# Optimization experiments

Hardware: AMD Instinct MI355X
Metric: run time of the kernel (lower is better)

## Reference

```python
import jax, jax.numpy as jnp
import numpy as np

# Static module configuration (RT-DETR defaults, 640x640 input pyramid)
SPATIAL_SHAPES = ((80, 80), (40, 40), (20, 20))
N_HEADS = 8
N_LEVELS = 3
N_POINTS = 4
D_MODEL = 256
HEAD_DIM = D_MODEL // N_HEADS
OFFSET_SCALE = 0.5
LP = N_LEVELS * N_POINTS


def setup_inputs() -> dict:
    key = jax.random.key(0)
    ks = jax.random.split(key, 10)
    B, Q = 16, 300
    S = sum(h * w for h, w in SPATIAL_SHAPES)  # 8400

    def w(k, shape, scale=0.02):
        return jax.random.normal(k, shape, jnp.float32) * scale

    return {
        "hidden_states": jax.random.normal(ks[0], (B, Q, D_MODEL), jnp.float32),
        "encoder_hidden_states": jax.random.normal(ks[1], (B, S, D_MODEL), jnp.float32),
        # (cx, cy, w, h) boxes in (0,1); 4-coordinate RTDETRv2 path
        "reference_points": jax.random.uniform(ks[2], (B, Q, 1, 4), jnp.float32, 0.1, 0.9),
        "w_value": w(ks[3], (D_MODEL, D_MODEL)),
        "b_value": jnp.zeros((D_MODEL,), jnp.float32),
        "w_offsets": w(ks[4], (N_HEADS * LP * 2, D_MODEL)),
        "b_offsets": w(ks[5], (N_HEADS * LP * 2,), 0.5),
        "w_attn": w(ks[6], (N_HEADS * LP, D_MODEL)),
        "b_attn": jnp.zeros((N_HEADS * LP,), jnp.float32),
        "w_out": w(ks[7], (D_MODEL, D_MODEL)),
        "b_out": jnp.zeros((D_MODEL,), jnp.float32),
    }


def _bilinear_sample(img, gx, gy):
    """grid_sample(mode=bilinear, padding_mode=zeros, align_corners=False).
    img: [N, C, H, W]; gx, gy: [N, Q, P] absolute pixel coords (already W*loc-0.5).
    Returns [N, Q, P, C]."""
    N, C, H, W = img.shape
    x0 = jnp.floor(gx)
    y0 = jnp.floor(gy)
    x1 = x0 + 1.0
    y1 = y0 + 1.0
    wx1 = gx - x0
    wx0 = 1.0 - wx1
    wy1 = gy - y0
    wy0 = 1.0 - wy1
    b = jnp.arange(N)[:, None, None]

    def gather(ix, iy):
        valid = (ix >= 0) & (ix < W) & (iy >= 0) & (iy < H)
        ixc = jnp.clip(ix, 0, W - 1).astype(jnp.int32)
        iyc = jnp.clip(iy, 0, H - 1).astype(jnp.int32)
        v = img[b, :, iyc, ixc]  # [N,Q,P,C]
        return v * valid[..., None].astype(img.dtype)

    return (gather(x0, y0) * (wx0 * wy0)[..., None]
            + gather(x1, y0) * (wx1 * wy0)[..., None]
            + gather(x0, y1) * (wx0 * wy1)[..., None]
            + gather(x1, y1) * (wx1 * wy1)[..., None])


def _msda_v2(hidden_states, encoder_hidden_states, reference_points,
             w_value, b_value, w_offsets, b_offsets, w_attn, b_attn, w_out, b_out):
    B, Q, _ = hidden_states.shape
    S = encoder_hidden_states.shape[1]

    value = (encoder_hidden_states @ w_value.T + b_value).reshape(B, S, N_HEADS, HEAD_DIM)
    offsets = (hidden_states @ w_offsets.T + b_offsets).reshape(B, Q, N_HEADS, LP, 2)
    attn = jax.nn.softmax(
        (hidden_states @ w_attn.T + b_attn).reshape(B, Q, N_HEADS, LP), axis=-1)

    # n_points_scale = [1/P]*L*P; 4-coordinate reference points (cx,cy,w,h)
    n_points_scale = jnp.float32(1.0 / N_POINTS)
    offset = offsets * n_points_scale * reference_points[:, :, None, :, 2:] * OFFSET_SCALE
    loc = reference_points[:, :, None, :, :2] + offset  # [B,Q,H,LP,2] in (0,1)

    # head-major value: [B*H, hd, S]
    v = value.transpose(0, 2, 3, 1).reshape(B * N_HEADS, HEAD_DIM, S)
    grids = loc.transpose(0, 2, 1, 3, 4).reshape(B * N_HEADS, Q, LP, 2)

    sampled = []
    start = 0
    for lvl, (H, W) in enumerate(SPATIAL_SHAPES):
        vl = v[:, :, start:start + H * W].reshape(B * N_HEADS, HEAD_DIM, H, W)
        g = grids[:, :, lvl * N_POINTS:(lvl + 1) * N_POINTS, :]
        # torch: grid = 2*loc-1 with align_corners=False -> pixel = loc*W - 0.5
        gx = g[..., 0] * W - 0.5
        gy = g[..., 1] * H - 0.5
        sampled.append(_bilinear_sample(vl, gx, gy))  # [B*H, Q, P, hd]
        start += H * W

    sv = jnp.concatenate(sampled, axis=2)  # [B*H, Q, LP, hd]
    aw = attn.transpose(0, 2, 1, 3).reshape(B * N_HEADS, Q, LP, 1)
    out = (sv * aw).sum(axis=2)  # [B*H, Q, hd]
    out = out.reshape(B, N_HEADS, Q, HEAD_DIM).transpose(0, 2, 1, 3).reshape(B, Q, D_MODEL)
    return out @ w_out.T + b_out


def reference(hidden_states, encoder_hidden_states, reference_points,
              w_value, b_value, w_offsets, b_offsets, w_attn, b_attn, w_out, b_out):
    return _msda_v2(hidden_states, encoder_hidden_states, reference_points,
                    w_value, b_value, w_offsets, b_offsets, w_attn, b_attn, w_out, b_out)
```

## Files before the change

kernel.cpp:

```cpp
#include <hip/hip_runtime.h>


typedef __attribute__((ext_vector_type(8))) short short8;
typedef __attribute__((ext_vector_type(4))) short short4v;
typedef __attribute__((ext_vector_type(4))) float f32x4;

__device__ __forceinline__ unsigned short f2bf(float f) {
    union { float f; unsigned int i; } v; v.f = f;
    unsigned int r = v.i + 0x7FFFu + ((v.i >> 16) & 1u);
    return (unsigned short)(r >> 16);
}
__device__ __forceinline__ float bf2f(unsigned short u) {
    union { unsigned int i; float f; } v;
    v.i = ((unsigned int)u) << 16;
    return v.f;
}
__device__ __forceinline__ short8 cvt8(const float* p) {
    f32x4 x = *(const f32x4*)p;
    f32x4 y = *(const f32x4*)(p + 4);
    short8 r;
#pragma unroll
    for (int q = 0; q < 4; ++q) {
        r[q]     = (short)f2bf(x[q]);
        r[q + 4] = (short)f2bf(y[q]);
    }
    return r;
}
__device__ __forceinline__ void barrier_lgkm() {
    asm volatile("s_waitcnt lgkmcnt(0)\n\ts_barrier" ::: "memory");
}

__global__ __launch_bounds__(256) void prep_kernel(
    const float* __restrict__ wv, const float* __restrict__ wo,
    const float* __restrict__ w_off, const float* __restrict__ w_attn,
    short8* __restrict__ wv_s, short8* __restrict__ wo_s, short8* __restrict__ wp_s)
{
    const int blk = blockIdx.x, tid = threadIdx.x;
    if (blk < 64) {
        const float* W = (blk < 32) ? wv : wo;
        short8* out    = (blk < 32) ? wv_s : wo_s;
        int s   = ((blk & 31) << 8) + tid;
        int kcb = s >> 10, sl = s & 1023;
        int n = ((sl >> 6) << 4) + (sl & 15);
        int k = (kcb << 5) + (((sl >> 4) & 3) << 3);
        out[s] = cvt8(W + n * 256 + k);
    } else {
        int s   = ((blk - 64) << 8) + tid;
        int kcb = s / 1152, sl = s - kcb * 1152;
        int n = ((sl >> 6) << 4) + (sl & 15);
        int k = (kcb << 5) + (((sl >> 4) & 3) << 3);
        const float* p = (n < 192) ? (w_off + (size_t)n * 256 + k)
                                   : (w_attn + (size_t)(n - 192) * 256 + k);
        wp_s[s] = cvt8(p);
    }
}

__global__ __launch_bounds__(256) void gemm128(
    const float* __restrict__ A,
    const short8* __restrict__ Wswz,
    const float* __restrict__ bias,
    unsigned short* __restrict__ C)
{
    __shared__ short8 lb[1024];
    const int tid  = threadIdx.x;
    const int wave = tid >> 6;
    const int lane = tid & 63;
    const int row0 = (blockIdx.x >> 1) * 128;
    const int colt = blockIdx.x & 1;
    const int mq   = wave >> 1;
    const int nq   = wave & 1;

    f32x4 acc[4][4];
#pragma unroll
    for (int i = 0; i < 4; ++i)
#pragma unroll
        for (int j = 0; j < 4; ++j) acc[i][j] = (f32x4){0.f, 0.f, 0.f, 0.f};

    const int sa0 = tid, sa1 = tid + 256;
    const int am0 = row0 + ((sa0 >> 6) << 4) + (sa0 & 15);
    const int ak0 = ((sa0 >> 4) & 3) << 3;
    const int am1 = row0 + ((sa1 >> 6) << 4) + (sa1 & 15);
    const int ak1 = ((sa1 >> 4) & 3) << 3;

    for (int kcb = 0; kcb < 8; ++kcb) {
        const int kc = kcb << 5;
        barrier_lgkm();
        lb[sa0] = cvt8(A + (size_t)am0 * 256 + kc + ak0);
        lb[sa1] = cvt8(A + (size_t)am1 * 256 + kc + ak1);
        const short8* wsrc = Wswz + (kcb << 10) + (colt << 9);
        lb[512 + tid]       = wsrc[tid];
        lb[768 + tid]       = wsrc[tid + 256];
        barrier_lgkm();

        short8 af[4], bf[4];
#pragma unroll
        for (int i = 0; i < 4; ++i) af[i] = lb[((mq << 2) + i) * 64 + lane];
#pragma unroll
        for (int j = 0; j < 4; ++j) bf[j] = lb[512 + ((nq << 2) + j) * 64 + lane];
#pragma unroll
        for (int i = 0; i < 4; ++i)
#pragma unroll
            for (int j = 0; j < 4; ++j)
                acc[i][j] = __builtin_amdgcn_mfma_f32_16x16x32_bf16(af[i], bf[j], acc[i][j], 0, 0, 0);
    }

    const int ncol = lane & 15;
    const int rsub = (lane >> 4) << 2;
#pragma unroll
    for (int i = 0; i < 4; ++i) {
        const int rb = row0 + ((mq << 2) + i) * 16 + rsub;
#pragma unroll
        for (int j = 0; j < 4; ++j) {
            const int n = (colt << 7) + ((nq << 2) + j) * 16 + ncol;
            const float bv = bias[n];
#pragma unroll
            for (int r = 0; r < 4; ++r)
                C[(size_t)(rb + r) * 256 + n] = f2bf(acc[i][j][r] + bv);
        }
    }
}

template <bool A_BF16, bool OUT_BF16>
__global__ __launch_bounds__(256) void gemm_nt(
    const void* __restrict__ Av,
    const short8* __restrict__ Wswz,
    const float* __restrict__ bias,
    void* __restrict__ Cv)
{
    __shared__ short8 lb[1024];
    const int tid  = threadIdx.x;
    const int wave = tid >> 6;
    const int lane = tid & 63;
    const int row0 = (blockIdx.x >> 1) * 64 + wave * 16;
    const int colt = blockIdx.x & 1;

    f32x4 acc[8];
#pragma unroll
    for (int t = 0; t < 8; ++t) acc[t] = (f32x4){0.f, 0.f, 0.f, 0.f};

    const int am = row0 + (lane & 15);
    const int kq = (lane >> 4) << 3;

    const unsigned short* Ab = (const unsigned short*)Av;
    const float*          Af = (const float*)Av;

    short8 acur[2], anext[2];
#pragma unroll
    for (int kk = 0; kk < 2; ++kk) {
        if (A_BF16) acur[kk] = *(const short8*)(Ab + (size_t)am * 256 + (kk << 5) + kq);
        else        acur[kk] = cvt8(Af + (size_t)am * 256 + (kk << 5) + kq);
    }

    for (int st = 0; st < 4; ++st) {
        barrier_lgkm();
#pragma unroll
        for (int i = 0; i < 4; ++i) {
            int s  = tid + (i << 8);
            int kk = s >> 9, r = s & 511;
            lb[s] = Wswz[(((st << 1) + kk) << 10) + (colt << 9) + r];
        }
        barrier_lgkm();

        if (st < 3) {
            int kc = (st + 1) << 6;
#pragma unroll
            for (int kk = 0; kk < 2; ++kk) {
                if (A_BF16) anext[kk] = *(const short8*)(Ab + (size_t)am * 256 + kc + (kk << 5) + kq);
                else        anext[kk] = cvt8(Af + (size_t)am * 256 + kc + (kk << 5) + kq);
            }
        }

#pragma unroll
        for (int t = 0; t < 8; ++t) {
            short8 b0 = lb[t * 64 + lane];
            acc[t] = __builtin_amdgcn_mfma_f32_16x16x32_bf16(acur[0], b0, acc[t], 0, 0, 0);
            short8 b1 = lb[512 + t * 64 + lane];
            acc[t] = __builtin_amdgcn_mfma_f32_16x16x32_bf16(acur[1], b1, acc[t], 0, 0, 0);
        }
        acur[0] = anext[0];
        acur[1] = anext[1];
    }

    const int ncol = lane & 15;
    const int rb   = row0 + ((lane >> 4) << 2);
#pragma unroll
    for (int t = 0; t < 8; ++t) {
        int n = (colt << 7) + (t << 4) + ncol;
        float bv = bias[n];
#pragma unroll
        for (int r = 0; r < 4; ++r) {
            float v = acc[t][r] + bv;
            if (OUT_BF16)
                ((unsigned short*)Cv)[(size_t)(rb + r) * 256 + n] = f2bf(v);
            else
                ((float*)Cv)[(size_t)(rb + r) * 256 + n] = v;
        }
    }
}

#define LGS 296
__global__ __launch_bounds__(256) void proj_gemm(
    const float* __restrict__ hidden,
    const short8* __restrict__ Wswz,
    const float* __restrict__ b_off, const float* __restrict__ b_attn,
    const float* __restrict__ refp,
    float* __restrict__ attnw, float* __restrict__ locw)
{
    __shared__ char smem[32 * LGS * 4];
    short8* lb = (short8*)smem;
    float*  lg = (float*)smem;

    const int tid  = threadIdx.x;
    const int wave = tid >> 6;
    const int lane = tid & 63;
    const int rq0  = blockIdx.x * 32;
    const int rg   = wave >> 1;
    const int ts   = (wave & 1) * 9;
    const int row0 = rq0 + rg * 16;

    f32x4 acc[9];
#pragma unroll
    for (int t = 0; t < 9; ++t) acc[t] = (f32x4){0.f, 0.f, 0.f, 0.f};

    const int am = row0 + (lane & 15);
    const int kq = (lane >> 4) << 3;

    for (int kcb = 0; kcb < 8; ++kcb) {
        __syncthreads();
#pragma unroll
        for (int i = 0; i < 5; ++i) {
            int s = tid + (i << 8);
            if (s < 1152) lb[s] = Wswz[kcb * 1152 + s];
        }
        __syncthreads();

        short8 a = cvt8(hidden + (size_t)am * 256 + (kcb << 5) + kq);
#pragma unroll
        for (int t = 0; t < 9; ++t)
            acc[t] = __builtin_amdgcn_mfma_f32_16x16x32_bf16(a, lb[(ts + t) * 64 + lane], acc[t], 0, 0, 0);
    }

    __syncthreads();
    const int ncol = lane & 15;
    const int rb   = rg * 16 + ((lane >> 4) << 2);
#pragma unroll
    for (int t = 0; t < 9; ++t) {
        int n = (ts + t) * 16 + ncol;
        float bv = (n < 192) ? b_off[n] : b_attn[n - 192];
#pragma unroll
        for (int r = 0; r < 4; ++r)
            lg[(rb + r) * LGS + n] = acc[t][r] + bv;
    }
    __syncthreads();

    {
        int r = tid >> 3, h = tid & 7;
        const float* lrow = lg + r * LGS + 192 + h * 12;
        float m = -1e30f;
#pragma unroll
        for (int p = 0; p < 12; ++p) m = fmaxf(m, lrow[p]);
        float e[12], sum = 0.f;
#pragma unroll
        for (int p = 0; p < 12; ++p) { e[p] = __expf(lrow[p] - m); sum += e[p]; }
        float inv = 1.f / sum;
        float* ao = attnw + (size_t)(rq0 + r) * 96 + h * 12;
#pragma unroll
        for (int p = 0; p < 12; ++p) ao[p] = e[p] * inv;
    }
    if (tid < 192) {
        int xy = tid & 1;
        for (int r = 0; r < 32; ++r) {
            int rq = rq0 + r;
            float rc  = refp[(size_t)rq * 4 + xy];
            float rwh = refp[(size_t)rq * 4 + 2 + xy];
            locw[(size_t)rq * 192 + tid] = rc + lg[r * LGS + tid] * 0.125f * rwh;
        }
    }
}

__global__ __launch_bounds__(256) void sample_kernel(
    const unsigned short* __restrict__ value,
    const float* __restrict__ attnw, const float* __restrict__ locw,
    unsigned short* __restrict__ sampled)
{
    const int rq0 = blockIdx.x << 2;
    const int tid = threadIdx.x;

    __shared__ int4   soff[4][96];
    __shared__ float4 swt[4][96];

    for (int it = tid; it < 384; it += 256) {
        int rsub = it / 96;
        int idx  = it - rsub * 96;
        int rq   = rq0 + rsub;
        int b    = rq / 300;
        int h  = idx / 12, lp = idx - h * 12;
        int l  = lp >> 2;
        int Wl = (l == 0) ? 80 : (l == 1) ? 40 : 20;
        int s0 = (l == 0) ? 0  : (l == 1) ? 6400 : 8000;
        float lx = locw[(size_t)rq * 192 + h * 24 + lp * 2];
        float ly = locw[(size_t)rq * 192 + h * 24 + lp * 2 + 1];
        float aw = attnw[(size_t)rq * 96 + h * 12 + lp];
        float gx = lx * (float)Wl - 0.5f;
        float gy = ly * (float)Wl - 0.5f;
        float x0f = floorf(gx), y0f = floorf(gy);
        int   x0 = (int)x0f,   y0 = (int)y0f;
        float wx1 = gx - x0f, wx0 = 1.f - wx1;
        float wy1 = gy - y0f, wy0 = 1.f - wy1;
        int4 of; float4 wt;
#pragma unroll
        for (int j = 0; j < 4; ++j) {
            int x = x0 + (j & 1), y = y0 + (j >> 1);
            bool ok = (x >= 0) & (x < Wl) & (y >= 0) & (y < Wl);
            int idx2 = ok ? (((b * 8400 + s0 + y * Wl + x) * 8 + h) * 32) : 0;
            float w = ok ? aw * ((j & 1) ? wx1 : wx0) * ((j >> 1) ? wy1 : wy0) : 0.f;
            ((int*)&of)[j] = idx2;
            ((float*)&wt)[j] = w;
        }
        soff[rsub][idx] = of;
        swt[rsub][idx]  = wt;
    }
    __syncthreads();

    const int rsub = tid >> 6;
    const int lane = tid & 63;
    const int h    = lane >> 3;
    const int cq   = (lane & 7) << 2;
    const int rq   = rq0 + rsub;

    float acc0 = 0.f, acc1 = 0.f, acc2 = 0.f, acc3 = 0.f;
    const int base = h * 12;
#pragma unroll
    for (int lp = 0; lp < 12; ++lp) {
        int4   of = soff[rsub][base + lp];
        float4 wt = swt[rsub][base + lp];
#pragma unroll
        for (int j = 0; j < 4; ++j) {
            int   o = ((const int*)&of)[j];
            float w = ((const float*)&wt)[j];
            uint2 u = *(const uint2*)(value + o + cq);
            union { unsigned int i; float f; } c0, c1, c2, c3;
            c0.i = u.x << 16; c1.i = u.x & 0xFFFF0000u;
            c2.i = u.y << 16; c3.i = u.y & 0xFFFF0000u;
            acc0 += w * c0.f; acc1 += w * c1.f;
            acc2 += w * c2.f; acc3 += w * c3.f;
        }
    }
    short4v out;
    out[0] = (short)f2bf(acc0);
    out[1] = (short)f2bf(acc1);
    out[2] = (short)f2bf(acc2);
    out[3] = (short)f2bf(acc3);
    *(short4v*)(sampled + (size_t)rq * 256 + h * 32 + cq) = out;
}

extern "C" void kernel_launch(void* const* d_in, const int* in_sizes, int n_in,
                              void* d_out, int out_size, void* d_ws, size_t ws_size,
                              hipStream_t stream)
{
    const float* hidden  = (const float*)d_in[0];
    const float* enc     = (const float*)d_in[1];
    const float* refp    = (const float*)d_in[2];
    const float* w_value = (const float*)d_in[3];
    const float* b_value = (const float*)d_in[4];
    const float* w_off   = (const float*)d_in[5];
    const float* b_off   = (const float*)d_in[6];
    const float* w_attn  = (const float*)d_in[7];
    const float* b_attn  = (const float*)d_in[8];
    const float* w_out   = (const float*)d_in[9];
    const float* b_out   = (const float*)d_in[10];

    char* ws = (char*)d_ws;
    unsigned short* value   = (unsigned short*)ws;
    unsigned short* sampled = (unsigned short*)(ws + 68812800);
    float*          attnw   = (float*)(ws + 71270400);
    float*          locw    = (float*)(ws + 73113600);
    short8*         wv_swz  = (short8*)(ws + 76800000);
    short8*         wo_swz  = (short8*)(ws + 76931072);
    short8*         wp_swz  = (short8*)(ws + 77062144);

    prep_kernel<<<100, 256, 0, stream>>>(w_value, w_out, w_off, w_attn,
                                         wv_swz, wo_swz, wp_swz);
    gemm128<<<2100, 256, 0, stream>>>(enc, wv_swz, b_value, value);
    proj_gemm<<<150, 256, 0, stream>>>(hidden, wp_swz, b_off, b_attn,
                                       refp, attnw, locw);
    sample_kernel<<<1200, 256, 0, stream>>>(value, attnw, locw, sampled);
    gemm_nt<true, false><<<150, 256, 0, stream>>>(sampled, wo_swz, b_out,
                                                  d_out);
}
```

Before: 289.8 us.

## Make value-projection GEMM persistent with LDS-resident weights and register-streamed A

The value-projection GEMM becomes a persistent kernel: 256 blocks of 512 threads each load the full swizzled bf16 weight matrix (128 KB) into LDS once via direct global-to-LDS loads. Each wave then loops over 32-row tiles, reading the fp32 activations straight into registers, converting them to bf16 in-register, and prefetching the next K chunks while issuing MFMAs. This removes the per-K-step LDS staging of A and the repeated weight reloads and barriers of the previous 2100-block kernel. The trade-off is low occupancy, since 128 KB of LDS allows one block per CU, and heavy register use, so hiding the latency of the A loads depends on the in-register prefetch.

```diff
diff --git a/kernel.cpp b/kernel.cpp
--- a/kernel.cpp
+++ b/kernel.cpp
@@ -26,8 +26,22 @@
     }
     return r;
 }
+__device__ __forceinline__ short8 pack8(f32x4 x, f32x4 y) {
+    short8 r;
+#pragma unroll
+    for (int q = 0; q < 4; ++q) {
+        r[q]     = (short)f2bf(x[q]);
+        r[q + 4] = (short)f2bf(y[q]);
+    }
+    return r;
+}
 __device__ __forceinline__ void barrier_lgkm() {
     asm volatile("s_waitcnt lgkmcnt(0)\n\ts_barrier" ::: "memory");
+}
+__device__ __forceinline__ void gload_lds16(const void* g, void* l) {
+    __builtin_amdgcn_global_load_lds(
+        (const __attribute__((address_space(1))) void*)g,
+        (__attribute__((address_space(3))) void*)l, 16, 0, 0);
 }
 
 __global__ __launch_bounds__(256) void prep_kernel(
@@ -55,67 +69,81 @@
     }
 }
 
-__global__ __launch_bounds__(256) void gemm128(
+__global__ __launch_bounds__(512) void gemm_value(
     const float* __restrict__ A,
     const short8* __restrict__ Wswz,
     const float* __restrict__ bias,
     unsigned short* __restrict__ C)
 {
-    __shared__ short8 lb[1024];
+    __shared__ short8 lb[8192];
     const int tid  = threadIdx.x;
     const int wave = tid >> 6;
     const int lane = tid & 63;
-    const int row0 = (blockIdx.x >> 1) * 128;
-    const int colt = blockIdx.x & 1;
-    const int mq   = wave >> 1;
-    const int nq   = wave & 1;
-
-    f32x4 acc[4][4];
-#pragma unroll
-    for (int i = 0; i < 4; ++i)
-#pragma unroll
-        for (int j = 0; j < 4; ++j) acc[i][j] = (f32x4){0.f, 0.f, 0.f, 0.f};
-
-    const int sa0 = tid, sa1 = tid + 256;
-    const int am0 = row0 + ((sa0 >> 6) << 4) + (sa0 & 15);
-    const int ak0 = ((sa0 >> 4) & 3) << 3;
-    const int am1 = row0 + ((sa1 >> 6) << 4) + (sa1 & 15);
-    const int ak1 = ((sa1 >> 4) & 3) << 3;
-
-    for (int kcb = 0; kcb < 8; ++kcb) {
-        const int kc = kcb << 5;
-        barrier_lgkm();
-        lb[sa0] = cvt8(A + (size_t)am0 * 256 + kc + ak0);
-        lb[sa1] = cvt8(A + (size_t)am1 * 256 + kc + ak1);
-        const short8* wsrc = Wswz + (kcb << 10) + (colt << 9);
-        lb[512 + tid]       = wsrc[tid];
-        lb[768 + tid]       = wsrc[tid + 256];
-        barrier_lgkm();
-
-        short8 af[4], bf[4];
-#pragma unroll
-        for (int i = 0; i < 4; ++i) af[i] = lb[((mq << 2) + i) * 64 + lane];
-#pragma unroll
-        for (int j = 0; j < 4; ++j) bf[j] = lb[512 + ((nq << 2) + j) * 64 + lane];
-#pragma unroll
-        for (int i = 0; i < 4; ++i)
-#pragma unroll
-            for (int j = 0; j < 4; ++j)
-                acc[i][j] = __builtin_amdgcn_mfma_f32_16x16x32_bf16(af[i], bf[j], acc[i][j], 0, 0, 0);
-    }
-
-    const int ncol = lane & 15;
-    const int rsub = (lane >> 4) << 2;
-#pragma unroll
-    for (int i = 0; i < 4; ++i) {
-        const int rb = row0 + ((mq << 2) + i) * 16 + rsub;
-#pragma unroll
-        for (int j = 0; j < 4; ++j) {
-            const int n = (colt << 7) + ((nq << 2) + j) * 16 + ncol;
-            const float bv = bias[n];
-#pragma unroll
-            for (int r = 0; r < 4; ++r)
-                C[(size_t)(rb + r) * 256 + n] = f2bf(acc[i][j][r] + bv);
+
+#pragma unroll
+    for (int r = 0; r < 16; ++r)
+        gload_lds16(Wswz + (r << 9) + (wave << 6) + lane,
+                    lb   + (r << 9) + (wave << 6));
+    asm volatile("s_waitcnt vmcnt(0)" ::: "memory");
+    __syncthreads();
+
+    const int ch  = wave & 1;
+    const int st  = (blockIdx.x << 2) + (wave >> 1);
+    const int rlo = lane & 15;
+    const int kq  = (lane >> 4) << 3;
+
+    for (int tile = st; tile < 4200; tile += 1024) {
+        const float* pa0 = A + (size_t)((tile << 5) + rlo) * 256 + kq;
+        const float* pa1 = pa0 + 16 * 256;
+
+        f32x4 acc[2][8];
+#pragma unroll
+        for (int i = 0; i < 2; ++i)
+#pragma unroll
+            for (int j = 0; j < 8; ++j) acc[i][j] = (f32x4){0.f, 0.f, 0.f, 0.f};
+
+        f32x4 a0[4][2], a1[4][2];
+#pragma unroll
+        for (int p = 0; p < 4; ++p) {
+            a0[p][0] = *(const f32x4*)(pa0 + (p << 5));
+            a0[p][1] = *(const f32x4*)(pa0 + (p << 5) + 4);
+            a1[p][0] = *(const f32x4*)(pa1 + (p << 5));
+            a1[p][1] = *(const f32x4*)(pa1 + (p << 5) + 4);
+        }
+
+#pragma unroll
+        for (int kcb = 0; kcb < 8; ++kcb) {
+            const int p = kcb & 3;
+            short8 af0 = pack8(a0[p][0], a0[p][1]);
+            short8 af1 = pack8(a1[p][0], a1[p][1]);
+            if (kcb < 4) {
+                const int ko = (kcb + 4) << 5;
+                a0[p][0] = *(const f32x4*)(pa0 + ko);
+                a0[p][1] = *(const f32x4*)(pa0 + ko + 4);
+                a1[p][0] = *(const f32x4*)(pa1 + ko);
+                a1[p][1] = *(const f32x4*)(pa1 + ko + 4);
+            }
+            const short8* bb = lb + (kcb << 10) + (ch << 9) + lane;
+#pragma unroll
+            for (int j = 0; j < 8; ++j) {
+                short8 bf = bb[(size_t)(j << 6)];
+                acc[0][j] = __builtin_amdgcn_mfma_f32_16x16x32_bf16(af0, bf, acc[0][j], 0, 0, 0);
+                acc[1][j] = __builtin_amdgcn_mfma_f32_16x16x32_bf16(af1, bf, acc[1][j], 0, 0, 0);
+            }
+        }
+
+        const int rsub = (lane >> 4) << 2;
+#pragma unroll
+        for (int i = 0; i < 2; ++i) {
+            const int rb = (tile << 5) + (i << 4) + rsub;
+#pragma unroll
+            for (int j = 0; j < 8; ++j) {
+                const int n = (ch << 7) + (j << 4) + rlo;
+                const float bv = bias[n];
+#pragma unroll
+                for (int r = 0; r < 4; ++r)
+                    C[(size_t)(rb + r) * 256 + n] = f2bf(acc[i][j][r] + bv);
+            }
         }
     }
 }
@@ -381,7 +409,7 @@
 
     prep_kernel<<<100, 256, 0, stream>>>(w_value, w_out, w_off, w_attn,
                                          wv_swz, wo_swz, wp_swz);
-    gemm128<<<2100, 256, 0, stream>>>(enc, wv_swz, b_value, value);
+    gemm_value<<<256, 512, 0, stream>>>(enc, wv_swz, b_value, value);
     proj_gemm<<<150, 256, 0, stream>>>(hidden, wp_swz, b_off, b_attn,
                                        refp, attnw, locw);
     sample_kernel<<<1200, 256, 0, stream>>>(value, attnw, locw, sampled);
```

After: 390.5 us. +34.8%, slower.

## Shrink projection and output GEMM tiles to 16 rows, read weights directly

Applied to the files above, without the earlier changes.

The offset/attention projection GEMM and the output GEMM now use 16-row blocks, which doubles the grid from 150 to 300 blocks. Each wave handles a slice of the output columns and reads the pre-swizzled bf16 weight fragments straight from global memory instead of staging them through LDS with barriers. This is meant to fill more of the GPU's compute units and remove the synchronisation in these small GEMMs. In exchange, weight reads become redundant across blocks and depend on the cache, and the load pipelining of the old gemm_nt is dropped.

```diff
diff --git a/kernel.cpp b/kernel.cpp
--- a/kernel.cpp
+++ b/kernel.cpp
@@ -120,84 +120,6 @@
     }
 }
 
-template <bool A_BF16, bool OUT_BF16>
-__global__ __launch_bounds__(256) void gemm_nt(
-    const void* __restrict__ Av,
-    const short8* __restrict__ Wswz,
-    const float* __restrict__ bias,
-    void* __restrict__ Cv)
-{
-    __shared__ short8 lb[1024];
-    const int tid  = threadIdx.x;
-    const int wave = tid >> 6;
-    const int lane = tid & 63;
-    const int row0 = (blockIdx.x >> 1) * 64 + wave * 16;
-    const int colt = blockIdx.x & 1;
-
-    f32x4 acc[8];
-#pragma unroll
-    for (int t = 0; t < 8; ++t) acc[t] = (f32x4){0.f, 0.f, 0.f, 0.f};
-
-    const int am = row0 + (lane & 15);
-    const int kq = (lane >> 4) << 3;
-
-    const unsigned short* Ab = (const unsigned short*)Av;
-    const float*          Af = (const float*)Av;
-
-    short8 acur[2], anext[2];
-#pragma unroll
-    for (int kk = 0; kk < 2; ++kk) {
-        if (A_BF16) acur[kk] = *(const short8*)(Ab + (size_t)am * 256 + (kk << 5) + kq);
-        else        acur[kk] = cvt8(Af + (size_t)am * 256 + (kk << 5) + kq);
-    }
-
-    for (int st = 0; st < 4; ++st) {
-        barrier_lgkm();
-#pragma unroll
-        for (int i = 0; i < 4; ++i) {
-            int s  = tid + (i << 8);
-            int kk = s >> 9, r = s & 511;
-            lb[s] = Wswz[(((st << 1) + kk) << 10) + (colt << 9) + r];
-        }
-        barrier_lgkm();
-
-        if (st < 3) {
-            int kc = (st + 1) << 6;
-#pragma unroll
-            for (int kk = 0; kk < 2; ++kk) {
-                if (A_BF16) anext[kk] = *(const short8*)(Ab + (size_t)am * 256 + kc + (kk << 5) + kq);
-                else        anext[kk] = cvt8(Af + (size_t)am * 256 + kc + (kk << 5) + kq);
-            }
-        }
-
-#pragma unroll
-        for (int t = 0; t < 8; ++t) {
-            short8 b0 = lb[t * 64 + lane];
-            acc[t] = __builtin_amdgcn_mfma_f32_16x16x32_bf16(acur[0], b0, acc[t], 0, 0, 0);
-            short8 b1 = lb[512 + t * 64 + lane];
-            acc[t] = __builtin_amdgcn_mfma_f32_16x16x32_bf16(acur[1], b1, acc[t], 0, 0, 0);
-        }
-        acur[0] = anext[0];
-        acur[1] = anext[1];
-    }
-
-    const int ncol = lane & 15;
-    const int rb   = row0 + ((lane >> 4) << 2);
-#pragma unroll
-    for (int t = 0; t < 8; ++t) {
-        int n = (colt << 7) + (t << 4) + ncol;
-        float bv = bias[n];
-#pragma unroll
-        for (int r = 0; r < 4; ++r) {
-            float v = acc[t][r] + bv;
-            if (OUT_BF16)
-                ((unsigned short*)Cv)[(size_t)(rb + r) * 256 + n] = f2bf(v);
-            else
-                ((float*)Cv)[(size_t)(rb + r) * 256 + n] = v;
-        }
-    }
-}
-
 #define LGS 296
 __global__ __launch_bounds__(256) void proj_gemm(
     const float* __restrict__ hidden,
@@ -206,54 +128,48 @@
     const float* __restrict__ refp,
     float* __restrict__ attnw, float* __restrict__ locw)
 {
-    __shared__ char smem[32 * LGS * 4];
-    short8* lb = (short8*)smem;
-    float*  lg = (float*)smem;
+    __shared__ float lg[16 * LGS];
 
     const int tid  = threadIdx.x;
     const int wave = tid >> 6;
     const int lane = tid & 63;
-    const int rq0  = blockIdx.x * 32;
-    const int rg   = wave >> 1;
-    const int ts   = (wave & 1) * 9;
-    const int row0 = rq0 + rg * 16;
-
-    f32x4 acc[9];
-#pragma unroll
-    for (int t = 0; t < 9; ++t) acc[t] = (f32x4){0.f, 0.f, 0.f, 0.f};
-
-    const int am = row0 + (lane & 15);
+    const int rq0  = blockIdx.x * 16;
+
+    const int ts = (wave < 2) ? wave * 5 : 10 + ((wave - 2) << 2);
+    const int tc = (wave < 2) ? 5 : 4;
+
+    f32x4 acc[5];
+#pragma unroll
+    for (int t = 0; t < 5; ++t) acc[t] = (f32x4){0.f, 0.f, 0.f, 0.f};
+
+    const int am = rq0 + (lane & 15);
     const int kq = (lane >> 4) << 3;
 
+#pragma unroll
     for (int kcb = 0; kcb < 8; ++kcb) {
-        __syncthreads();
-#pragma unroll
-        for (int i = 0; i < 5; ++i) {
-            int s = tid + (i << 8);
-            if (s < 1152) lb[s] = Wswz[kcb * 1152 + s];
-        }
-        __syncthreads();
-
         short8 a = cvt8(hidden + (size_t)am * 256 + (kcb << 5) + kq);
-#pragma unroll
-        for (int t = 0; t < 9; ++t)
-            acc[t] = __builtin_amdgcn_mfma_f32_16x16x32_bf16(a, lb[(ts + t) * 64 + lane], acc[t], 0, 0, 0);
-    }
-
+        const short8* bb = Wswz + kcb * 1152 + (ts << 6) + lane;
+#pragma unroll
+        for (int t = 0; t < 5; ++t)
+            if (t < tc)
+                acc[t] = __builtin_amdgcn_mfma_f32_16x16x32_bf16(a, bb[t << 6], acc[t], 0, 0, 0);
+    }
+
+    const int ncol = lane & 15;
+    const int rb   = (lane >> 4) << 2;
+#pragma unroll
+    for (int t = 0; t < 5; ++t) {
+        if (t < tc) {
+            int n = ((ts + t) << 4) + ncol;
+            float bv = (n < 192) ? b_off[n] : b_attn[n - 192];
+#pragma unroll
+            for (int r = 0; r < 4; ++r)
+                lg[(rb + r) * LGS + n] = acc[t][r] + bv;
+        }
+    }
     __syncthreads();
-    const int ncol = lane & 15;
-    const int rb   = rg * 16 + ((lane >> 4) << 2);
-#pragma unroll
-    for (int t = 0; t < 9; ++t) {
-        int n = (ts + t) * 16 + ncol;
-        float bv = (n < 192) ? b_off[n] : b_attn[n - 192];
-#pragma unroll
-        for (int r = 0; r < 4; ++r)
-            lg[(rb + r) * LGS + n] = acc[t][r] + bv;
-    }
-    __syncthreads();
-
-    {
+
+    if (tid < 128) {
         int r = tid >> 3, h = tid & 7;
         const float* lrow = lg + r * LGS + 192 + h * 12;
         float m = -1e30f;
@@ -269,12 +185,52 @@
     }
     if (tid < 192) {
         int xy = tid & 1;
-        for (int r = 0; r < 32; ++r) {
+#pragma unroll
+        for (int r = 0; r < 16; ++r) {
             int rq = rq0 + r;
             float rc  = refp[(size_t)rq * 4 + xy];
             float rwh = refp[(size_t)rq * 4 + 2 + xy];
             locw[(size_t)rq * 192 + tid] = rc + lg[r * LGS + tid] * 0.125f * rwh;
         }
+    }
+}
+
+__global__ __launch_bounds__(256) void out_gemm(
+    const unsigned short* __restrict__ Ab,
+    const short8* __restrict__ Wswz,
+    const float* __restrict__ bias,
+    float* __restrict__ Cv)
+{
+    const int tid  = threadIdx.x;
+    const int wave = tid >> 6;
+    const int lane = tid & 63;
+    const int row0 = blockIdx.x * 16;
+
+    f32x4 acc[4];
+#pragma unroll
+    for (int t = 0; t < 4; ++t) acc[t] = (f32x4){0.f, 0.f, 0.f, 0.f};
+
+    const int am = row0 + (lane & 15);
+    const int kq = (lane >> 4) << 3;
+
+#pragma unroll
+    for (int kcb = 0; kcb < 8; ++kcb) {
+        short8 a = *(const short8*)(Ab + (size_t)am * 256 + (kcb << 5) + kq);
+        const short8* bb = Wswz + (kcb << 10) + (wave << 8) + lane;
+#pragma unroll
+        for (int t = 0; t < 4; ++t)
+            acc[t] = __builtin_amdgcn_mfma_f32_16x16x32_bf16(a, bb[t << 6], acc[t], 0, 0, 0);
+    }
+
+    const int ncol = lane & 15;
+    const int rb   = row0 + ((lane >> 4) << 2);
+#pragma unroll
+    for (int t = 0; t < 4; ++t) {
+        int n = (wave << 6) + (t << 4) + ncol;
+        float bv = bias[n];
+#pragma unroll
+        for (int r = 0; r < 4; ++r)
+            Cv[(size_t)(rb + r) * 256 + n] = acc[t][r] + bv;
     }
 }
 
@@ -382,9 +338,8 @@
     prep_kernel<<<100, 256, 0, stream>>>(w_value, w_out, w_off, w_attn,
                                          wv_swz, wo_swz, wp_swz);
     gemm128<<<2100, 256, 0, stream>>>(enc, wv_swz, b_value, value);
-    proj_gemm<<<150, 256, 0, stream>>>(hidden, wp_swz, b_off, b_attn,
+    proj_gemm<<<300, 256, 0, stream>>>(hidden, wp_swz, b_off, b_attn,
                                        refp, attnw, locw);
     sample_kernel<<<1200, 256, 0, stream>>>(value, attnw, locw, sampled);
-    gemm_nt<true, false><<<150, 256, 0, stream>>>(sampled, wo_swz, b_out,
-                                                  d_out);
-}
+    out_gemm<<<300, 256, 0, stream>>>(sampled, wo_swz, b_out, (float*)d_out);
+}
```

After: 280.3 us. 3.3% less time.
